# Optimization experiments

Measured on AMD Instinct MI355X. Metric: run time of the kernel, lower is better.

The kernel has to match this reference:

```python
import jax, jax.numpy as jnp
import numpy as np

NUM_TOKENS = 1024  # max_num_tokens = ori_indexes.max()+1; fixed for jit (indexes drawn in [0,1024))


def setup_inputs() -> dict:
    key = jax.random.key(0)
    k1, k2 = jax.random.split(key)
    hidden = jax.random.normal(k1, (8, 2048, 768), dtype=jnp.float32)
    ori_indexes = jnp.sort(
        jax.random.randint(k2, (8, 2048), 0, NUM_TOKENS, dtype=jnp.int64), axis=-1
    )
    return {"hidden": hidden, "ori_indexes": ori_indexes}


def reference(hidden, ori_indexes):
    # mode='mean': sum sub-token vectors per original token, divide by count (clamped >=1).
    # Equivalent to the torch mask+bmm path, but as a direct segment reduction.
    def agg_one(h, idx):  # h: [S, D], idx: [S]
        summed = jax.ops.segment_sum(h, idx, num_segments=NUM_TOKENS)            # [T, D]
        counts = jax.ops.segment_sum(jnp.ones(idx.shape, h.dtype), idx,
                                     num_segments=NUM_TOKENS)                    # [T]
        return summed / jnp.clip(counts, 1.0)[:, None]
    return jax.vmap(agg_one)(hidden, ori_indexes)  # [B, T, D]
```

## Files before the change

### kernel.cpp

```cpp
#include <hip/hip_runtime.h>
#include <hip/hip_bf16.h>


#define SGA_B 8
#define SGA_S 2048
#define SGA_D 768
#define SGA_T 1024
#define SGA_NV (SGA_D / 4)

typedef float f32x4 __attribute__((ext_vector_type(4)));

__global__ __launch_bounds__(256) void sga_segmean_kernel(
    const float* __restrict__ hidden,
    const int* __restrict__ idx,
    float* __restrict__ out) {
    const int b = blockIdx.y;
    const int wid = threadIdx.x >> 6;
    const int lane = threadIdx.x & 63;
    const int t = blockIdx.x * 4 + wid;

    const int* __restrict__ ib = idx + b * SGA_S;

    int lo = 0, hi = SGA_S;
    while (lo < hi) { int m = (lo + hi) >> 1; if (ib[m] < t) lo = m + 1; else hi = m; }
    const int s0 = lo;
    hi = SGA_S;
    while (lo < hi) { int m = (lo + hi) >> 1; if (ib[m] < t + 1) lo = m + 1; else hi = m; }
    const int s1 = lo;

    const f32x4* __restrict__ hbase =
        reinterpret_cast<const f32x4*>(hidden) + (size_t)b * SGA_S * SGA_NV + lane;

    f32x4 a0 = (f32x4)0.f, a1 = (f32x4)0.f, a2 = (f32x4)0.f;

    int s = s0;
    for (; s + 1 < s1; s += 2) {
        const f32x4* r0 = hbase + (size_t)s * SGA_NV;
        const f32x4* r1 = r0 + SGA_NV;
        f32x4 v00 = __builtin_nontemporal_load(r0);
        f32x4 v01 = __builtin_nontemporal_load(r0 + 64);
        f32x4 v02 = __builtin_nontemporal_load(r0 + 128);
        f32x4 v10 = __builtin_nontemporal_load(r1);
        f32x4 v11 = __builtin_nontemporal_load(r1 + 64);
        f32x4 v12 = __builtin_nontemporal_load(r1 + 128);
        a0 += v00; a1 += v01; a2 += v02;
        a0 += v10; a1 += v11; a2 += v12;
    }
    if (s < s1) {
        const f32x4* r0 = hbase + (size_t)s * SGA_NV;
        a0 += __builtin_nontemporal_load(r0);
        a1 += __builtin_nontemporal_load(r0 + 64);
        a2 += __builtin_nontemporal_load(r0 + 128);
    }

    const int cnt = s1 - s0;
    const float inv = (cnt > 0) ? (1.0f / (float)cnt) : 0.0f;
    a0 *= inv; a1 *= inv; a2 *= inv;

    f32x4* __restrict__ obase =
        reinterpret_cast<f32x4*>(out) + ((size_t)b * SGA_T + t) * SGA_NV + lane;
    __builtin_nontemporal_store(a0, obase);
    __builtin_nontemporal_store(a1, obase + 64);
    __builtin_nontemporal_store(a2, obase + 128);
}

extern "C" void kernel_launch(void* const* d_in, const int* in_sizes, int n_in,
                              void* d_out, int out_size, void* d_ws, size_t ws_size,
                              hipStream_t stream) {
    const float* hidden = (const float*)d_in[0];
    const int* idx = (const int*)d_in[1];
    float* out = (float*)d_out;

    dim3 grid(SGA_T / 4, SGA_B, 1);
    sga_segmean_kernel<<<grid, dim3(256, 1, 1), 0, stream>>>(hidden, idx, out);
}
```

Before: 19.80 us.

## Assign segments to waves by start row instead of by output token

Each wave still zero-fills its own token if that token is empty. The segment-reduction work is now keyed by input row pairs: a wave owns rows 2w and 2w+1, and for any row that starts a new segment it scans forward to the segment end, averages the rows and writes to that token's output. This ties the work distribution to where segments begin rather than to a binary search per token, though segment lengths still vary. It adds a serial scan of the index array per segment start and keeps the two binary searches.

```diff
diff --git a/kernel.cpp b/kernel.cpp
--- a/kernel.cpp
+++ b/kernel.cpp
@@ -15,53 +15,68 @@
     const int* __restrict__ idx,
     float* __restrict__ out) {
     const int b = blockIdx.y;
-    const int wid = threadIdx.x >> 6;
+    const int w = blockIdx.x * 4 + (threadIdx.x >> 6);
     const int lane = threadIdx.x & 63;
-    const int t = blockIdx.x * 4 + wid;
 
     const int* __restrict__ ib = idx + b * SGA_S;
 
+    const f32x4* __restrict__ hbase =
+        reinterpret_cast<const f32x4*>(hidden) + (size_t)b * SGA_S * SGA_NV + lane;
+    f32x4* __restrict__ obat =
+        reinterpret_cast<f32x4*>(out) + (size_t)b * SGA_T * SGA_NV + lane;
+
     int lo = 0, hi = SGA_S;
-    while (lo < hi) { int m = (lo + hi) >> 1; if (ib[m] < t) lo = m + 1; else hi = m; }
+    while (lo < hi) { int m = (lo + hi) >> 1; if (ib[m] < w) lo = m + 1; else hi = m; }
     const int s0 = lo;
     hi = SGA_S;
-    while (lo < hi) { int m = (lo + hi) >> 1; if (ib[m] < t + 1) lo = m + 1; else hi = m; }
-    const int s1 = lo;
-
-    const f32x4* __restrict__ hbase =
-        reinterpret_cast<const f32x4*>(hidden) + (size_t)b * SGA_S * SGA_NV + lane;
-
-    f32x4 a0 = (f32x4)0.f, a1 = (f32x4)0.f, a2 = (f32x4)0.f;
-
-    int s = s0;
-    for (; s + 1 < s1; s += 2) {
-        const f32x4* r0 = hbase + (size_t)s * SGA_NV;
-        const f32x4* r1 = r0 + SGA_NV;
-        f32x4 v00 = __builtin_nontemporal_load(r0);
-        f32x4 v01 = __builtin_nontemporal_load(r0 + 64);
-        f32x4 v02 = __builtin_nontemporal_load(r0 + 128);
-        f32x4 v10 = __builtin_nontemporal_load(r1);
-        f32x4 v11 = __builtin_nontemporal_load(r1 + 64);
-        f32x4 v12 = __builtin_nontemporal_load(r1 + 128);
-        a0 += v00; a1 += v01; a2 += v02;
-        a0 += v10; a1 += v11; a2 += v12;
-    }
-    if (s < s1) {
-        const f32x4* r0 = hbase + (size_t)s * SGA_NV;
-        a0 += __builtin_nontemporal_load(r0);
-        a1 += __builtin_nontemporal_load(r0 + 64);
-        a2 += __builtin_nontemporal_load(r0 + 128);
+    while (lo < hi) { int m = (lo + hi) >> 1; if (ib[m] < w + 1) lo = m + 1; else hi = m; }
+    if (s0 == lo) {
+        f32x4 z = (f32x4)0.f;
+        f32x4* o = obat + (size_t)w * SGA_NV;
+        __builtin_nontemporal_store(z, o);
+        __builtin_nontemporal_store(z, o + 64);
+        __builtin_nontemporal_store(z, o + 128);
     }
 
-    const int cnt = s1 - s0;
-    const float inv = (cnt > 0) ? (1.0f / (float)cnt) : 0.0f;
-    a0 *= inv; a1 *= inv; a2 *= inv;
+    const int r0 = 2 * w;
+#pragma unroll
+    for (int rr = r0; rr < r0 + 2; ++rr) {
+        const int t = ib[rr];
+        const int p = (rr == 0) ? -1 : ib[rr - 1];
+        if (t != p) {
+            int e = rr + 1;
+            while (e < SGA_S && ib[e] == t) ++e;
 
-    f32x4* __restrict__ obase =
-        reinterpret_cast<f32x4*>(out) + ((size_t)b * SGA_T + t) * SGA_NV + lane;
-    __builtin_nontemporal_store(a0, obase);
-    __builtin_nontemporal_store(a1, obase + 64);
-    __builtin_nontemporal_store(a2, obase + 128);
+            f32x4 a0 = (f32x4)0.f, a1 = (f32x4)0.f, a2 = (f32x4)0.f;
+            int s = rr;
+            for (; s + 1 < e; s += 2) {
+                const f32x4* r0p = hbase + (size_t)s * SGA_NV;
+                const f32x4* r1p = r0p + SGA_NV;
+                f32x4 v00 = __builtin_nontemporal_load(r0p);
+                f32x4 v01 = __builtin_nontemporal_load(r0p + 64);
+                f32x4 v02 = __builtin_nontemporal_load(r0p + 128);
+                f32x4 v10 = __builtin_nontemporal_load(r1p);
+                f32x4 v11 = __builtin_nontemporal_load(r1p + 64);
+                f32x4 v12 = __builtin_nontemporal_load(r1p + 128);
+                a0 += v00; a1 += v01; a2 += v02;
+                a0 += v10; a1 += v11; a2 += v12;
+            }
+            if (s < e) {
+                const f32x4* rp = hbase + (size_t)s * SGA_NV;
+                a0 += __builtin_nontemporal_load(rp);
+                a1 += __builtin_nontemporal_load(rp + 64);
+                a2 += __builtin_nontemporal_load(rp + 128);
+            }
+
+            const float inv = 1.0f / (float)(e - rr);
+            a0 *= inv; a1 *= inv; a2 *= inv;
+
+            f32x4* o = obat + (size_t)t * SGA_NV;
+            __builtin_nontemporal_store(a0, o);
+            __builtin_nontemporal_store(a1, o + 64);
+            __builtin_nontemporal_store(a2, o + 128);
+        }
+    }
 }
 
 extern "C" void kernel_launch(void* const* d_in, const int* in_sizes, int n_in,
```

Result: slower. 22.39 us (+13.1%).

## Replace static token-per-wave grid with persistent atomic work queue per batch

Applied to the files above, without the earlier changes.

Adds a persistent-style kernel where each wave pulls token indices from a per-batch atomic counter in workspace, so load imbalance from uneven segment lengths is spread dynamically. A memset of the counters is launched before the kernel each call. The static kernel is kept as a fallback when no workspace is provided. This adds an extra memset launch and atomic contention on 8 counters.

```diff
diff --git a/kernel.cpp b/kernel.cpp
--- a/kernel.cpp
+++ b/kernel.cpp
@@ -7,10 +7,71 @@
 #define SGA_D 768
 #define SGA_T 1024
 #define SGA_NV (SGA_D / 4)
+#define SGA_CTR_STRIDE 32
 
 typedef float f32x4 __attribute__((ext_vector_type(4)));
 
-__global__ __launch_bounds__(256) void sga_segmean_kernel(
+__global__ __launch_bounds__(256) void sga_queue_kernel(
+    const float* __restrict__ hidden,
+    const int* __restrict__ idx,
+    float* __restrict__ out,
+    int* __restrict__ ctrs) {
+    const int lane = threadIdx.x & 63;
+    const int b = blockIdx.x & 7;
+    int* ctr = ctrs + b * SGA_CTR_STRIDE;
+
+    const int* __restrict__ ib = idx + b * SGA_S;
+    const f32x4* __restrict__ hbase =
+        reinterpret_cast<const f32x4*>(hidden) + (size_t)b * SGA_S * SGA_NV + lane;
+    f32x4* __restrict__ obat =
+        reinterpret_cast<f32x4*>(out) + (size_t)b * SGA_T * SGA_NV + lane;
+
+    for (;;) {
+        int t;
+        if (lane == 0) t = atomicAdd(ctr, 1);
+        t = __shfl(t, 0);
+        if (t >= SGA_T) break;
+
+        int lo = 0, hi = SGA_S;
+        while (lo < hi) { int m = (lo + hi) >> 1; if (ib[m] < t) lo = m + 1; else hi = m; }
+        const int s0 = lo;
+        hi = SGA_S;
+        while (lo < hi) { int m = (lo + hi) >> 1; if (ib[m] < t + 1) lo = m + 1; else hi = m; }
+        const int s1 = lo;
+
+        f32x4 a0 = (f32x4)0.f, a1 = (f32x4)0.f, a2 = (f32x4)0.f;
+        int s = s0;
+        for (; s + 1 < s1; s += 2) {
+            const f32x4* r0 = hbase + (size_t)s * SGA_NV;
+            const f32x4* r1 = r0 + SGA_NV;
+            f32x4 v00 = __builtin_nontemporal_load(r0);
+            f32x4 v01 = __builtin_nontemporal_load(r0 + 64);
+            f32x4 v02 = __builtin_nontemporal_load(r0 + 128);
+            f32x4 v10 = __builtin_nontemporal_load(r1);
+            f32x4 v11 = __builtin_nontemporal_load(r1 + 64);
+            f32x4 v12 = __builtin_nontemporal_load(r1 + 128);
+            a0 += v00; a1 += v01; a2 += v02;
+            a0 += v10; a1 += v11; a2 += v12;
+        }
+        if (s < s1) {
+            const f32x4* rp = hbase + (size_t)s * SGA_NV;
+            a0 += __builtin_nontemporal_load(rp);
+            a1 += __builtin_nontemporal_load(rp + 64);
+            a2 += __builtin_nontemporal_load(rp + 128);
+        }
+
+        const int cnt = s1 - s0;
+        const float inv = (cnt > 0) ? (1.0f / (float)cnt) : 0.0f;
+        a0 *= inv; a1 *= inv; a2 *= inv;
+
+        f32x4* o = obat + (size_t)t * SGA_NV;
+        __builtin_nontemporal_store(a0, o);
+        __builtin_nontemporal_store(a1, o + 64);
+        __builtin_nontemporal_store(a2, o + 128);
+    }
+}
+
+__global__ __launch_bounds__(256) void sga_static_kernel(
     const float* __restrict__ hidden,
     const int* __restrict__ idx,
     float* __restrict__ out) {
@@ -18,50 +79,39 @@
     const int wid = threadIdx.x >> 6;
     const int lane = threadIdx.x & 63;
     const int t = blockIdx.x * 4 + wid;
-
     const int* __restrict__ ib = idx + b * SGA_S;
-
     int lo = 0, hi = SGA_S;
     while (lo < hi) { int m = (lo + hi) >> 1; if (ib[m] < t) lo = m + 1; else hi = m; }
     const int s0 = lo;
     hi = SGA_S;
     while (lo < hi) { int m = (lo + hi) >> 1; if (ib[m] < t + 1) lo = m + 1; else hi = m; }
     const int s1 = lo;
-
     const f32x4* __restrict__ hbase =
         reinterpret_cast<const f32x4*>(hidden) + (size_t)b * SGA_S * SGA_NV + lane;
-
     f32x4 a0 = (f32x4)0.f, a1 = (f32x4)0.f, a2 = (f32x4)0.f;
-
     int s = s0;
     for (; s + 1 < s1; s += 2) {
         const f32x4* r0 = hbase + (size_t)s * SGA_NV;
         const f32x4* r1 = r0 + SGA_NV;
-        f32x4 v00 = __builtin_nontemporal_load(r0);
-        f32x4 v01 = __builtin_nontemporal_load(r0 + 64);
-        f32x4 v02 = __builtin_nontemporal_load(r0 + 128);
-        f32x4 v10 = __builtin_nontemporal_load(r1);
-        f32x4 v11 = __builtin_nontemporal_load(r1 + 64);
-        f32x4 v12 = __builtin_nontemporal_load(r1 + 128);
-        a0 += v00; a1 += v01; a2 += v02;
-        a0 += v10; a1 += v11; a2 += v12;
-    }
-    if (s < s1) {
-        const f32x4* r0 = hbase + (size_t)s * SGA_NV;
         a0 += __builtin_nontemporal_load(r0);
         a1 += __builtin_nontemporal_load(r0 + 64);
         a2 += __builtin_nontemporal_load(r0 + 128);
+        a0 += __builtin_nontemporal_load(r1);
+        a1 += __builtin_nontemporal_load(r1 + 64);
+        a2 += __builtin_nontemporal_load(r1 + 128);
     }
-
-    const int cnt = s1 - s0;
-    const float inv = (cnt > 0) ? (1.0f / (float)cnt) : 0.0f;
+    if (s < s1) {
+        const f32x4* rp = hbase + (size_t)s * SGA_NV;
+        a0 += __builtin_nontemporal_load(rp);
+        a1 += __builtin_nontemporal_load(rp + 64);
+        a2 += __builtin_nontemporal_load(rp + 128);
+    }
+    const float inv = (s1 > s0) ? (1.0f / (float)(s1 - s0)) : 0.0f;
     a0 *= inv; a1 *= inv; a2 *= inv;
-
-    f32x4* __restrict__ obase =
-        reinterpret_cast<f32x4*>(out) + ((size_t)b * SGA_T + t) * SGA_NV + lane;
-    __builtin_nontemporal_store(a0, obase);
-    __builtin_nontemporal_store(a1, obase + 64);
-    __builtin_nontemporal_store(a2, obase + 128);
+    f32x4* o = reinterpret_cast<f32x4*>(out) + ((size_t)b * SGA_T + t) * SGA_NV + lane;
+    __builtin_nontemporal_store(a0, o);
+    __builtin_nontemporal_store(a1, o + 64);
+    __builtin_nontemporal_store(a2, o + 128);
 }
 
 extern "C" void kernel_launch(void* const* d_in, const int* in_sizes, int n_in,
@@ -71,6 +121,14 @@
     const int* idx = (const int*)d_in[1];
     float* out = (float*)d_out;
 
-    dim3 grid(SGA_T / 4, SGA_B, 1);
-    sga_segmean_kernel<<<grid, dim3(256, 1, 1), 0, stream>>>(hidden, idx, out);
+    const size_t ctr_bytes = (size_t)SGA_B * SGA_CTR_STRIDE * sizeof(int);
+    if (d_ws != nullptr && ws_size >= ctr_bytes) {
+        int* ctrs = (int*)d_ws;
+        hipMemsetAsync(ctrs, 0, ctr_bytes, stream);
+        sga_queue_kernel<<<dim3(2048, 1, 1), dim3(256, 1, 1), 0, stream>>>(
+            hidden, idx, out, ctrs);
+    } else {
+        sga_static_kernel<<<dim3(SGA_T / 4, SGA_B, 1), dim3(256, 1, 1), 0, stream>>>(
+            hidden, idx, out);
+    }
 }
```

Result: slower. 45.59 us (+130.2%).
